# Kernel tuning notes

Hardware: AMD Instinct MI355X
Metric: run time of the kernel (lower is better)

Reference implementation:

```python
import jax, jax.numpy as jnp
import numpy as np

DIM = 1024
N_HEADS = 16
HEAD_DIM = DIM // N_HEADS
D_LATENT = 256
B, T = 1, 4096


def setup_inputs() -> dict:
    key = jax.random.key(0)
    ks = jax.random.split(key, 6)
    s = 0.02
    return {
        "x": jax.random.normal(ks[0], (B, T, DIM), dtype=jnp.float32),
        "W_DKV": jax.random.normal(ks[1], (DIM, D_LATENT), dtype=jnp.float32) * s,
        "W_UK": jax.random.normal(ks[2], (D_LATENT, DIM), dtype=jnp.float32) * s,
        "W_UV": jax.random.normal(ks[3], (D_LATENT, DIM), dtype=jnp.float32) * s,
        "W_UQ": jax.random.normal(ks[4], (DIM, DIM), dtype=jnp.float32) * s,
        "W_O": jax.random.normal(ks[5], (DIM, DIM), dtype=jnp.float32) * s,
    }


def reference(x, W_DKV, W_UK, W_UV, W_UQ, W_O):
    b, t, d = x.shape
    h, hd = N_HEADS, HEAD_DIM
    # low-rank latent KV projection
    c_kv = x @ W_DKV                                   # (b, t, d_latent)
    k = (c_kv @ W_UK).reshape(b, t, h, hd)             # (b, t, h, hd)
    v = (c_kv @ W_UV).reshape(b, t, h, hd)
    q = (x @ W_UQ).reshape(b, t, h, hd)
    scale = 1.0 / jnp.sqrt(jnp.asarray(hd, x.dtype))
    scores = jnp.einsum("bqhd,bkhd->bhqk", q, k) * scale   # (b, h, t, t)
    causal = jnp.tril(jnp.ones((t, t), dtype=bool))
    scores = jnp.where(causal, scores, jnp.asarray(-jnp.inf, scores.dtype))
    probs = jax.nn.softmax(scores, axis=-1)            # dropout is eval-mode identity
    ctx = jnp.einsum("bhqk,bkhd->bqhd", probs, v).reshape(b, t, d)
    return ctx @ W_O
```

## Files before the change

kernel.cpp:

```cpp
#include <hip/hip_runtime.h>
#include <hip/hip_bf16.h>
#include <stdint.h>

#define T_SEQ 4096
#define DIMX 1024
#define NH 16
#define HD 64
#define DLAT 256

typedef __bf16 bf16x8 __attribute__((ext_vector_type(8)));
typedef float floatx4 __attribute__((ext_vector_type(4)));

#define MFMA(a, b, c) __builtin_amdgcn_mfma_f32_16x16x32_bf16(a, b, c, 0, 0, 0)

__global__ __launch_bounds__(256) void prep_kernel(
    const float* __restrict__ x, const float* __restrict__ wdkv,
    const float* __restrict__ wuk, const float* __restrict__ wuv,
    const float* __restrict__ wuq, const float* __restrict__ wo,
    __bf16* __restrict__ x_bf, __bf16* __restrict__ wt_dkv,
    __bf16* __restrict__ wt_uk, __bf16* __restrict__ wt_uv,
    __bf16* __restrict__ wt_uq, __bf16* __restrict__ wt_o) {
  int id = blockIdx.x;
  if (id < 2048) {
    int i = id * 256 + threadIdx.x;
    const float4* p = (const float4*)x;
    float4 a = p[2 * i], b = p[2 * i + 1];
    bf16x8 r = {(__bf16)a.x, (__bf16)a.y, (__bf16)a.z, (__bf16)a.w,
                (__bf16)b.x, (__bf16)b.y, (__bf16)b.z, (__bf16)b.w};
    *(bf16x8*)(x_bf + 8 * (size_t)i) = r;
    return;
  }
  int t = id - 2048;
  const float* in;
  __bf16* out;
  int R, C, lt;
  if (t < 64)       { in = wdkv; out = wt_dkv; R = 1024; C = 256;  lt = t; }
  else if (t < 128) { in = wuk;  out = wt_uk;  R = 256;  C = 1024; lt = t - 64; }
  else if (t < 192) { in = wuv;  out = wt_uv;  R = 256;  C = 1024; lt = t - 128; }
  else if (t < 448) { in = wuq;  out = wt_uq;  R = 1024; C = 1024; lt = t - 192; }
  else              { in = wo;   out = wt_o;   R = 1024; C = 1024; lt = t - 448; }
  __shared__ __bf16 tls[64][65];
  int tpr = C >> 6;
  int r0 = (lt / tpr) * 64, c0 = (lt % tpr) * 64;
  int tid = threadIdx.x;
#pragma unroll
  for (int i = 0; i < 16; i++) {
    int idx = tid + i * 256;
    int r = idx >> 6, c = idx & 63;
    tls[r][c] = (__bf16)in[(size_t)(r0 + r) * C + c0 + c];
  }
  __syncthreads();
#pragma unroll
  for (int i = 0; i < 16; i++) {
    int idx = tid + i * 256;
    int rr = idx & 63, cc = idx >> 6;
    out[(size_t)(c0 + cc) * R + r0 + rr] = tls[rr][cc];
  }
}

#define ASTR 56
__global__ __launch_bounds__(256) void gemm_a(const __bf16* __restrict__ A,
                                              const __bf16* __restrict__ B1,
                                              const __bf16* __restrict__ B2,
                                              __bf16* __restrict__ C1,
                                              __bf16* __restrict__ C2) {
  __shared__ __attribute__((aligned(16))) __bf16 Al[64 * ASTR];
  __shared__ __attribute__((aligned(16))) __bf16 Bl[64 * ASTR];
  int tid = threadIdx.x;
  int wave = tid >> 6, lane = tid & 63;
  int quad = lane >> 4, l16 = lane & 15;
  int bx = blockIdx.x, m0 = blockIdx.y * 64;
  const __bf16* Bt;
  __bf16* C;
  int n0, N;
  float sc;
  if (bx < 4) { Bt = B1; C = C1; n0 = bx * 64; N = DLAT; sc = 1.0f; }
  else        { Bt = B2; C = C2; n0 = (bx - 4) * 64; N = DIMX; sc = 0.125f; }
  int srow = tid >> 2, skc = (tid & 3) << 3;
  const int K = DIMX;

  floatx4 acc[4];
#pragma unroll
  for (int i = 0; i < 4; i++) acc[i] = (floatx4){0.f, 0.f, 0.f, 0.f};
  const __bf16* Ap = A + (size_t)(m0 + srow) * K + skc;
  const __bf16* Bp = Bt + (size_t)(n0 + srow) * K + skc;
  for (int k0 = 0; k0 < K; k0 += 32) {
    *(bf16x8*)&Al[srow * ASTR + skc] = *(const bf16x8*)(Ap + k0);
    *(bf16x8*)&Bl[srow * ASTR + skc] = *(const bf16x8*)(Bp + k0);
    __syncthreads();
    bf16x8 af = *(const bf16x8*)&Al[(wave * 16 + l16) * ASTR + quad * 8];
#pragma unroll
    for (int nt = 0; nt < 4; nt++) {
      bf16x8 bfr = *(const bf16x8*)&Bl[(nt * 16 + l16) * ASTR + quad * 8];
      acc[nt] = MFMA(af, bfr, acc[nt]);
    }
    __syncthreads();
  }
#pragma unroll
  for (int nt = 0; nt < 4; nt++)
#pragma unroll
    for (int r = 0; r < 4; r++) {
      int row = m0 + wave * 16 + quad * 4 + r;
      int col = n0 + nt * 16 + l16;
      C[(size_t)row * N + col] = (__bf16)(acc[nt][r] * sc);
    }
}

__global__ __launch_bounds__(256) void gemm_kv(const __bf16* __restrict__ A,
                                               const __bf16* __restrict__ Bk,
                                               const __bf16* __restrict__ Bv,
                                               __bf16* __restrict__ k,
                                               __bf16* __restrict__ vt) {
  __shared__ __attribute__((aligned(16))) __bf16 Al[64 * ASTR];
  __shared__ __attribute__((aligned(16))) __bf16 Bl[64 * ASTR];
  __shared__ __attribute__((aligned(16))) __bf16 tt[64 * 72];
  int tid = threadIdx.x;
  int wave = tid >> 6, lane = tid & 63;
  int quad = lane >> 4, l16 = lane & 15;
  int bx = blockIdx.x, m0 = blockIdx.y * 64;
  bool is_k = (bx < 16);
  const __bf16* Bt = is_k ? Bk : Bv;
  int n0 = (is_k ? bx : bx - 16) * 64;
  int srow = tid >> 2, skc = (tid & 3) << 3;
  const int K = DLAT;

  floatx4 acc[4];
#pragma unroll
  for (int i = 0; i < 4; i++) acc[i] = (floatx4){0.f, 0.f, 0.f, 0.f};
  const __bf16* Ap = A + (size_t)(m0 + srow) * K + skc;
  const __bf16* Bp = Bt + (size_t)(n0 + srow) * K + skc;
  for (int k0 = 0; k0 < K; k0 += 32) {
    *(bf16x8*)&Al[srow * ASTR + skc] = *(const bf16x8*)(Ap + k0);
    *(bf16x8*)&Bl[srow * ASTR + skc] = *(const bf16x8*)(Bp + k0);
    __syncthreads();
    bf16x8 af = *(const bf16x8*)&Al[(wave * 16 + l16) * ASTR + quad * 8];
#pragma unroll
    for (int nt = 0; nt < 4; nt++) {
      bf16x8 bfr = *(const bf16x8*)&Bl[(nt * 16 + l16) * ASTR + quad * 8];
      acc[nt] = MFMA(af, bfr, acc[nt]);
    }
    __syncthreads();
  }
  if (is_k) {
#pragma unroll
    for (int nt = 0; nt < 4; nt++)
#pragma unroll
      for (int r = 0; r < 4; r++) {
        int row = m0 + wave * 16 + quad * 4 + r;
        int col = n0 + nt * 16 + l16;
        k[(size_t)row * DIMX + col] = (__bf16)acc[nt][r];
      }
  } else {
#pragma unroll
    for (int nt = 0; nt < 4; nt++)
#pragma unroll
      for (int r = 0; r < 4; r++)
        tt[(nt * 16 + l16) * 72 + wave * 16 + quad * 4 + r] = (__bf16)acc[nt][r];
    __syncthreads();
#pragma unroll
    for (int i = 0; i < 2; i++) {
      int idx = tid + i * 256;
      int cc = idx >> 3, rr = (idx & 7) << 3;
      *(bf16x8*)&vt[(size_t)(n0 + cc) * T_SEQ + m0 + rr] =
          *(const bf16x8*)&tt[cc * 72 + rr];
    }
  }
}

#define PST 72
__global__ __launch_bounds__(512, 4) void mla_attn5(const __bf16* __restrict__ Q,
                                                    const __bf16* __restrict__ Kg,
                                                    const __bf16* __restrict__ Vt,
                                                    __bf16* __restrict__ ctx) {
  __shared__ __attribute__((aligned(16))) __bf16 Kl[2][64 * 64];
  __shared__ __attribute__((aligned(16))) __bf16 Vl[2][64 * 64];
  __shared__ __attribute__((aligned(16))) __bf16 Pl[128 * PST];
  int tid = threadIdx.x;
  int wave = tid >> 6, lane = tid & 63;
  int quad = lane >> 4, l16 = lane & 15;
  int wq = wave & 3;
  bool isA = (wave < 4);
  int qa = blockIdx.x, h = blockIdx.y;
  int qb = 63 - qa;
  int myqt = isA ? qa : qb;
  int myq0 = myqt * 64;
  int srow = tid >> 3, pos = tid & 7;
  int gco = pos << 3;
  int sw = ((pos ^ (srow & 7)) << 3);
  int swr = srow * 64 + sw;

  *(bf16x8*)&Pl[srow * PST + gco] =
      *(const bf16x8*)&Q[(size_t)(qa * 64 + srow) * DIMX + h * HD + gco];
  *(bf16x8*)&Pl[(64 + srow) * PST + gco] =
      *(const bf16x8*)&Q[(size_t)(qb * 64 + srow) * DIMX + h * HD + gco];
  *(bf16x8*)&Kl[0][swr] =
      *(const bf16x8*)&Kg[(size_t)srow * DIMX + h * HD + gco];
  *(bf16x8*)&Vl[0][swr] =
      *(const bf16x8*)&Vt[(size_t)(h * HD + srow) * T_SEQ + gco];
  __syncthreads();
  int fr = (wave * 16 + l16) * PST;
  bf16x8 qf0 = *(const bf16x8*)&Pl[fr + quad * 8];
  bf16x8 qf1 = *(const bf16x8*)&Pl[fr + 32 + quad * 8];

  int c0s = ((quad ^ (l16 & 7)) << 3);
  int c1s = (((4 + quad) ^ (l16 & 7)) << 3);

  floatx4 o[4];
  float l_i[4];
#pragma unroll
  for (int i = 0; i < 4; i++) {
    o[i] = (floatx4){0.f, 0.f, 0.f, 0.f};
    l_i[i] = 0.f;
  }

  for (int kt = 0; kt <= qb; kt++) {
    int cur = kt & 1, nxt = cur ^ 1;
    bool pre = (kt < qb);
    bf16x8 kpre, vpre;
    if (pre) {
      int k0n = (kt + 1) * 64;
      kpre = *(const bf16x8*)&Kg[(size_t)(k0n + srow) * DIMX + h * HD + gco];
      vpre = *(const bf16x8*)&Vt[(size_t)(h * HD + srow) * T_SEQ + k0n + gco];
    }
    if (!isA || kt <= qa) {
      const __bf16* Kc = Kl[cur];
      const __bf16* Vc = Vl[cur];
      floatx4 s[4];
#pragma unroll
      for (int ct = 0; ct < 4; ct++) {
        int rb = (ct * 16 + l16) * 64;
        bf16x8 kf0 = *(const bf16x8*)&Kc[rb + c0s];
        bf16x8 kf1 = *(const bf16x8*)&Kc[rb + c1s];
        floatx4 z = (floatx4){0.f, 0.f, 0.f, 0.f};
        z = MFMA(qf0, kf0, z);
        z = MFMA(qf1, kf1, z);
        s[ct] = z;
      }
      bool diag = (kt == myqt);
#pragma unroll
      for (int ct = 0; ct < 4; ct++)
#pragma unroll
        for (int r = 0; r < 4; r++) {
          float p = __expf(s[ct][r]);
          if (diag && (ct * 16 + l16 > wq * 16 + quad * 4 + r)) p = 0.f;
          l_i[r] += p;
          Pl[(wave * 16 + quad * 4 + r) * PST + ct * 16 + l16] = (__bf16)p;
        }
      bf16x8 pf0 = *(const bf16x8*)&Pl[fr + quad * 8];
      bf16x8 pf1 = *(const bf16x8*)&Pl[fr + 32 + quad * 8];
#pragma unroll
      for (int dt = 0; dt < 4; dt++) {
        int rb = (dt * 16 + l16) * 64;
        bf16x8 vf0 = *(const bf16x8*)&Vc[rb + c0s];
        bf16x8 vf1 = *(const bf16x8*)&Vc[rb + c1s];
        o[dt] = MFMA(pf0, vf0, o[dt]);
        o[dt] = MFMA(pf1, vf1, o[dt]);
      }
    }
    if (pre) {
      *(bf16x8*)&Kl[nxt][swr] = kpre;
      *(bf16x8*)&Vl[nxt][swr] = vpre;
    }
    __syncthreads();
  }

#pragma unroll
  for (int off = 1; off < 16; off <<= 1)
#pragma unroll
    for (int r = 0; r < 4; r++) l_i[r] += __shfl_xor(l_i[r], off, 64);

#pragma unroll
  for (int dt = 0; dt < 4; dt++)
#pragma unroll
    for (int r = 0; r < 4; r++) {
      float val = o[dt][r] / l_i[r];
      int row = myq0 + wq * 16 + quad * 4 + r;
      int col = h * HD + dt * 16 + l16;
      ctx[(size_t)row * DIMX + col] = (__bf16)val;
    }
}

__global__ __launch_bounds__(256) void gemm_f(const __bf16* __restrict__ A,
                                              const __bf16* __restrict__ Bt,
                                              float* __restrict__ C,
                                              int M, int N, int K) {
  __shared__ __attribute__((aligned(16))) __bf16 Al[64 * ASTR];
  __shared__ __attribute__((aligned(16))) __bf16 Bl[64 * ASTR];
  int tid = threadIdx.x;
  int wave = tid >> 6, lane = tid & 63;
  int quad = lane >> 4, l16 = lane & 15;
  int n0 = blockIdx.x * 64, m0 = blockIdx.y * 64;
  int srow = tid >> 2, skc = (tid & 3) << 3;

  floatx4 acc[4];
#pragma unroll
  for (int i = 0; i < 4; i++) acc[i] = (floatx4){0.f, 0.f, 0.f, 0.f};
  const __bf16* Ap = A + (size_t)(m0 + srow) * K + skc;
  const __bf16* Bp = Bt + (size_t)(n0 + srow) * K + skc;
  for (int k0 = 0; k0 < K; k0 += 32) {
    *(bf16x8*)&Al[srow * ASTR + skc] = *(const bf16x8*)(Ap + k0);
    *(bf16x8*)&Bl[srow * ASTR + skc] = *(const bf16x8*)(Bp + k0);
    __syncthreads();
    bf16x8 af = *(const bf16x8*)&Al[(wave * 16 + l16) * ASTR + quad * 8];
#pragma unroll
    for (int nt = 0; nt < 4; nt++) {
      bf16x8 bfr = *(const bf16x8*)&Bl[(nt * 16 + l16) * ASTR + quad * 8];
      acc[nt] = MFMA(af, bfr, acc[nt]);
    }
    __syncthreads();
  }
#pragma unroll
  for (int nt = 0; nt < 4; nt++)
#pragma unroll
    for (int r = 0; r < 4; r++) {
      int row = m0 + wave * 16 + quad * 4 + r;
      int col = n0 + nt * 16 + l16;
      C[(size_t)row * N + col] = acc[nt][r];
    }
}

extern "C" void kernel_launch(void* const* d_in, const int* in_sizes, int n_in,
                              void* d_out, int out_size, void* d_ws,
                              size_t ws_size, hipStream_t stream) {
  const float* x = (const float*)d_in[0];
  const float* wdkv = (const float*)d_in[1];
  const float* wuk = (const float*)d_in[2];
  const float* wuv = (const float*)d_in[3];
  const float* wuq = (const float*)d_in[4];
  const float* wo = (const float*)d_in[5];
  float* out = (float*)d_out;

  __bf16* ws = (__bf16*)d_ws;
  __bf16* x_bf = ws;
  __bf16* q = x_bf + (size_t)T_SEQ * DIMX;
  __bf16* k = q + (size_t)T_SEQ * DIMX;
  __bf16* vt = k + (size_t)T_SEQ * DIMX;
  __bf16* ctx = vt + (size_t)T_SEQ * DIMX;
  __bf16* ckv = ctx + (size_t)T_SEQ * DIMX;
  __bf16* wt_dkv = ckv + (size_t)T_SEQ * DLAT;
  __bf16* wt_uk = wt_dkv + (size_t)DLAT * DIMX;
  __bf16* wt_uv = wt_uk + (size_t)DIMX * DLAT;
  __bf16* wt_uq = wt_uv + (size_t)DIMX * DLAT;
  __bf16* wt_o = wt_uq + (size_t)DIMX * DIMX;

  dim3 blk(256);
  prep_kernel<<<dim3(2752), blk, 0, stream>>>(x, wdkv, wuk, wuv, wuq, wo, x_bf,
                                              wt_dkv, wt_uk, wt_uv, wt_uq, wt_o);
  gemm_a<<<dim3(20, T_SEQ / 64), blk, 0, stream>>>(x_bf, wt_dkv, wt_uq, ckv, q);
  gemm_kv<<<dim3(32, T_SEQ / 64), blk, 0, stream>>>(ckv, wt_uk, wt_uv, k, vt);
  mla_attn5<<<dim3(32, NH), dim3(512), 0, stream>>>(q, k, vt, ctx);
  gemm_f<<<dim3(DIMX / 64, T_SEQ / 64), blk, 0, stream>>>(ctx, wt_o, out, T_SEQ,
                                                          DIMX, DIMX);
}
```

Baseline: 230.2 us.

## Retile projection GEMMs to 128x128 with direct global-to-LDS loads

Replaces the 64x64-tile GEMMs for the latent/query, K/V and output projections with 128x128 tiles where each wave computes a 64x64 sub-tile via 16 MFMAs per k-step. Operand tiles are staged with global_load_lds, bypassing registers. The aim is more arithmetic reuse per loaded byte and fewer load instructions. It also reverses the query-tile order for half the heads in the attention kernel to spread causal work, at the cost of unpadded LDS (possible bank conflicts), more registers and fewer blocks per grid.

```diff
diff --git a/kernel.cpp b/kernel.cpp
--- a/kernel.cpp
+++ b/kernel.cpp
@@ -12,6 +12,12 @@
 typedef float floatx4 __attribute__((ext_vector_type(4)));
 
 #define MFMA(a, b, c) __builtin_amdgcn_mfma_f32_16x16x32_bf16(a, b, c, 0, 0, 0)
+
+__device__ inline void gload_lds16(const __bf16* g, __bf16* l) {
+  __builtin_amdgcn_global_load_lds(
+      (const __attribute__((address_space(1))) uint32_t*)g,
+      (__attribute__((address_space(3))) uint32_t*)l, 16, 0, 0);
+}
 
 __global__ __launch_bounds__(256) void prep_kernel(
     const float* __restrict__ x, const float* __restrict__ wdkv,
@@ -58,113 +64,200 @@
   }
 }
 
-#define ASTR 56
-__global__ __launch_bounds__(256) void gemm_a(const __bf16* __restrict__ A,
-                                              const __bf16* __restrict__ B1,
-                                              const __bf16* __restrict__ B2,
-                                              __bf16* __restrict__ C1,
-                                              __bf16* __restrict__ C2) {
-  __shared__ __attribute__((aligned(16))) __bf16 Al[64 * ASTR];
-  __shared__ __attribute__((aligned(16))) __bf16 Bl[64 * ASTR];
+
+__global__ __launch_bounds__(256) void gemm_a128(const __bf16* __restrict__ A,
+                                                 const __bf16* __restrict__ B1,
+                                                 const __bf16* __restrict__ B2,
+                                                 __bf16* __restrict__ C1,
+                                                 __bf16* __restrict__ C2) {
+  __shared__ __attribute__((aligned(16))) __bf16 Al[128 * 32];
+  __shared__ __attribute__((aligned(16))) __bf16 Bl[128 * 32];
   int tid = threadIdx.x;
-  int wave = tid >> 6, lane = tid & 63;
+  int w = tid >> 6, lane = tid & 63;
   int quad = lane >> 4, l16 = lane & 15;
-  int bx = blockIdx.x, m0 = blockIdx.y * 64;
+  int mw = w & 1, nw = w >> 1;
+  int bx = blockIdx.x, m0 = blockIdx.y * 128;
   const __bf16* Bt;
   __bf16* C;
   int n0, N;
   float sc;
-  if (bx < 4) { Bt = B1; C = C1; n0 = bx * 64; N = DLAT; sc = 1.0f; }
-  else        { Bt = B2; C = C2; n0 = (bx - 4) * 64; N = DIMX; sc = 0.125f; }
-  int srow = tid >> 2, skc = (tid & 3) << 3;
+  if (bx < 2) { Bt = B1; C = C1; n0 = bx * 128; N = DLAT; sc = 1.0f; }
+  else        { Bt = B2; C = C2; n0 = (bx - 2) * 128; N = DIMX; sc = 0.125f; }
   const int K = DIMX;
-
-  floatx4 acc[4];
-#pragma unroll
-  for (int i = 0; i < 4; i++) acc[i] = (floatx4){0.f, 0.f, 0.f, 0.f};
-  const __bf16* Ap = A + (size_t)(m0 + srow) * K + skc;
-  const __bf16* Bp = Bt + (size_t)(n0 + srow) * K + skc;
+  int arow = w * 32 + (lane >> 2), acol = (lane & 3) << 3;
+
+  floatx4 acc[4][4];
+#pragma unroll
+  for (int i = 0; i < 4; i++)
+#pragma unroll
+    for (int j = 0; j < 4; j++) acc[i][j] = (floatx4){0.f, 0.f, 0.f, 0.f};
+
   for (int k0 = 0; k0 < K; k0 += 32) {
-    *(bf16x8*)&Al[srow * ASTR + skc] = *(const bf16x8*)(Ap + k0);
-    *(bf16x8*)&Bl[srow * ASTR + skc] = *(const bf16x8*)(Bp + k0);
-    __syncthreads();
-    bf16x8 af = *(const bf16x8*)&Al[(wave * 16 + l16) * ASTR + quad * 8];
-#pragma unroll
-    for (int nt = 0; nt < 4; nt++) {
-      bf16x8 bfr = *(const bf16x8*)&Bl[(nt * 16 + l16) * ASTR + quad * 8];
-      acc[nt] = MFMA(af, bfr, acc[nt]);
-    }
-    __syncthreads();
-  }
-#pragma unroll
-  for (int nt = 0; nt < 4; nt++)
-#pragma unroll
-    for (int r = 0; r < 4; r++) {
-      int row = m0 + wave * 16 + quad * 4 + r;
-      int col = n0 + nt * 16 + l16;
-      C[(size_t)row * N + col] = (__bf16)(acc[nt][r] * sc);
-    }
-}
-
-__global__ __launch_bounds__(256) void gemm_kv(const __bf16* __restrict__ A,
-                                               const __bf16* __restrict__ Bk,
-                                               const __bf16* __restrict__ Bv,
-                                               __bf16* __restrict__ k,
-                                               __bf16* __restrict__ vt) {
-  __shared__ __attribute__((aligned(16))) __bf16 Al[64 * ASTR];
-  __shared__ __attribute__((aligned(16))) __bf16 Bl[64 * ASTR];
-  __shared__ __attribute__((aligned(16))) __bf16 tt[64 * 72];
+#pragma unroll
+    for (int j = 0; j < 2; j++) {
+      gload_lds16(A + (size_t)(m0 + arow + j * 16) * K + k0 + acol,
+                  &Al[(w * 32 + j * 16) * 32]);
+      gload_lds16(Bt + (size_t)(n0 + arow + j * 16) * K + k0 + acol,
+                  &Bl[(w * 32 + j * 16) * 32]);
+    }
+    __syncthreads();
+    bf16x8 af[4], bfr[4];
+#pragma unroll
+    for (int mt = 0; mt < 4; mt++)
+      af[mt] = *(const bf16x8*)&Al[(mw * 64 + mt * 16 + l16) * 32 + quad * 8];
+#pragma unroll
+    for (int nt = 0; nt < 4; nt++)
+      bfr[nt] = *(const bf16x8*)&Bl[(nw * 64 + nt * 16 + l16) * 32 + quad * 8];
+#pragma unroll
+    for (int mt = 0; mt < 4; mt++)
+#pragma unroll
+      for (int nt = 0; nt < 4; nt++)
+        acc[mt][nt] = MFMA(af[mt], bfr[nt], acc[mt][nt]);
+    __syncthreads();
+  }
+#pragma unroll
+  for (int mt = 0; mt < 4; mt++)
+#pragma unroll
+    for (int nt = 0; nt < 4; nt++)
+#pragma unroll
+      for (int r = 0; r < 4; r++) {
+        int row = m0 + mw * 64 + mt * 16 + quad * 4 + r;
+        int col = n0 + nw * 64 + nt * 16 + l16;
+        C[(size_t)row * N + col] = (__bf16)(acc[mt][nt][r] * sc);
+      }
+}
+
+__global__ __launch_bounds__(256) void gemm_kv128(const __bf16* __restrict__ A,
+                                                  const __bf16* __restrict__ Bk,
+                                                  const __bf16* __restrict__ Bv,
+                                                  __bf16* __restrict__ k,
+                                                  __bf16* __restrict__ vt) {
+  __shared__ __attribute__((aligned(16))) __bf16 Al[128 * 32];
+  __shared__ __attribute__((aligned(16))) __bf16 Bl[128 * 32];
+  __shared__ __attribute__((aligned(16))) __bf16 tw[4][64 * 72];
   int tid = threadIdx.x;
-  int wave = tid >> 6, lane = tid & 63;
+  int w = tid >> 6, lane = tid & 63;
   int quad = lane >> 4, l16 = lane & 15;
-  int bx = blockIdx.x, m0 = blockIdx.y * 64;
-  bool is_k = (bx < 16);
+  int mw = w & 1, nw = w >> 1;
+  int bx = blockIdx.x, m0 = blockIdx.y * 128;
+  bool is_k = (bx < 8);
   const __bf16* Bt = is_k ? Bk : Bv;
-  int n0 = (is_k ? bx : bx - 16) * 64;
-  int srow = tid >> 2, skc = (tid & 3) << 3;
+  int n0 = (is_k ? bx : bx - 8) * 128;
   const int K = DLAT;
-
-  floatx4 acc[4];
-#pragma unroll
-  for (int i = 0; i < 4; i++) acc[i] = (floatx4){0.f, 0.f, 0.f, 0.f};
-  const __bf16* Ap = A + (size_t)(m0 + srow) * K + skc;
-  const __bf16* Bp = Bt + (size_t)(n0 + srow) * K + skc;
+  int arow = w * 32 + (lane >> 2), acol = (lane & 3) << 3;
+
+  floatx4 acc[4][4];
+#pragma unroll
+  for (int i = 0; i < 4; i++)
+#pragma unroll
+    for (int j = 0; j < 4; j++) acc[i][j] = (floatx4){0.f, 0.f, 0.f, 0.f};
+
   for (int k0 = 0; k0 < K; k0 += 32) {
-    *(bf16x8*)&Al[srow * ASTR + skc] = *(const bf16x8*)(Ap + k0);
-    *(bf16x8*)&Bl[srow * ASTR + skc] = *(const bf16x8*)(Bp + k0);
-    __syncthreads();
-    bf16x8 af = *(const bf16x8*)&Al[(wave * 16 + l16) * ASTR + quad * 8];
-#pragma unroll
-    for (int nt = 0; nt < 4; nt++) {
-      bf16x8 bfr = *(const bf16x8*)&Bl[(nt * 16 + l16) * ASTR + quad * 8];
-      acc[nt] = MFMA(af, bfr, acc[nt]);
-    }
+#pragma unroll
+    for (int j = 0; j < 2; j++) {
+      gload_lds16(A + (size_t)(m0 + arow + j * 16) * K + k0 + acol,
+                  &Al[(w * 32 + j * 16) * 32]);
+      gload_lds16(Bt + (size_t)(n0 + arow + j * 16) * K + k0 + acol,
+                  &Bl[(w * 32 + j * 16) * 32]);
+    }
+    __syncthreads();
+    bf16x8 af[4], bfr[4];
+#pragma unroll
+    for (int mt = 0; mt < 4; mt++)
+      af[mt] = *(const bf16x8*)&Al[(mw * 64 + mt * 16 + l16) * 32 + quad * 8];
+#pragma unroll
+    for (int nt = 0; nt < 4; nt++)
+      bfr[nt] = *(const bf16x8*)&Bl[(nw * 64 + nt * 16 + l16) * 32 + quad * 8];
+#pragma unroll
+    for (int mt = 0; mt < 4; mt++)
+#pragma unroll
+      for (int nt = 0; nt < 4; nt++)
+        acc[mt][nt] = MFMA(af[mt], bfr[nt], acc[mt][nt]);
     __syncthreads();
   }
   if (is_k) {
 #pragma unroll
+    for (int mt = 0; mt < 4; mt++)
+#pragma unroll
+      for (int nt = 0; nt < 4; nt++)
+#pragma unroll
+        for (int r = 0; r < 4; r++) {
+          int row = m0 + mw * 64 + mt * 16 + quad * 4 + r;
+          int col = n0 + nw * 64 + nt * 16 + l16;
+          k[(size_t)row * DIMX + col] = (__bf16)acc[mt][nt][r];
+        }
+  } else {
+#pragma unroll
+    for (int mt = 0; mt < 4; mt++)
+#pragma unroll
+      for (int nt = 0; nt < 4; nt++)
+#pragma unroll
+        for (int r = 0; r < 4; r++)
+          tw[w][(nt * 16 + l16) * 72 + mt * 16 + quad * 4 + r] =
+              (__bf16)acc[mt][nt][r];
+    int cbase = lane >> 3, chunk = lane & 7;
+#pragma unroll
+    for (int i = 0; i < 8; i++) {
+      int c = cbase + i * 8;
+      bf16x8 v8 = *(const bf16x8*)&tw[w][c * 72 + chunk * 8];
+      *(bf16x8*)&vt[(size_t)(n0 + nw * 64 + c) * T_SEQ + m0 + mw * 64 +
+                    chunk * 8] = v8;
+    }
+  }
+}
+
+__global__ __launch_bounds__(256) void gemm_f128(const __bf16* __restrict__ A,
+                                                 const __bf16* __restrict__ Bt,
+                                                 float* __restrict__ C) {
+  __shared__ __attribute__((aligned(16))) __bf16 Al[128 * 32];
+  __shared__ __attribute__((aligned(16))) __bf16 Bl[128 * 32];
+  int tid = threadIdx.x;
+  int w = tid >> 6, lane = tid & 63;
+  int quad = lane >> 4, l16 = lane & 15;
+  int mw = w & 1, nw = w >> 1;
+  int n0 = blockIdx.x * 128, m0 = blockIdx.y * 128;
+  const int K = DIMX, N = DIMX;
+  int arow = w * 32 + (lane >> 2), acol = (lane & 3) << 3;
+
+  floatx4 acc[4][4];
+#pragma unroll
+  for (int i = 0; i < 4; i++)
+#pragma unroll
+    for (int j = 0; j < 4; j++) acc[i][j] = (floatx4){0.f, 0.f, 0.f, 0.f};
+
+  for (int k0 = 0; k0 < K; k0 += 32) {
+#pragma unroll
+    for (int j = 0; j < 2; j++) {
+      gload_lds16(A + (size_t)(m0 + arow + j * 16) * K + k0 + acol,
+                  &Al[(w * 32 + j * 16) * 32]);
+      gload_lds16(Bt + (size_t)(n0 + arow + j * 16) * K + k0 + acol,
+                  &Bl[(w * 32 + j * 16) * 32]);
+    }
+    __syncthreads();
+    bf16x8 af[4], bfr[4];
+#pragma unroll
+    for (int mt = 0; mt < 4; mt++)
+      af[mt] = *(const bf16x8*)&Al[(mw * 64 + mt * 16 + l16) * 32 + quad * 8];
+#pragma unroll
     for (int nt = 0; nt < 4; nt++)
+      bfr[nt] = *(const bf16x8*)&Bl[(nw * 64 + nt * 16 + l16) * 32 + quad * 8];
+#pragma unroll
+    for (int mt = 0; mt < 4; mt++)
+#pragma unroll
+      for (int nt = 0; nt < 4; nt++)
+        acc[mt][nt] = MFMA(af[mt], bfr[nt], acc[mt][nt]);
+    __syncthreads();
+  }
+#pragma unroll
+  for (int mt = 0; mt < 4; mt++)
+#pragma unroll
+    for (int nt = 0; nt < 4; nt++)
 #pragma unroll
       for (int r = 0; r < 4; r++) {
-        int row = m0 + wave * 16 + quad * 4 + r;
-        int col = n0 + nt * 16 + l16;
-        k[(size_t)row * DIMX + col] = (__bf16)acc[nt][r];
+        int row = m0 + mw * 64 + mt * 16 + quad * 4 + r;
+        int col = n0 + nw * 64 + nt * 16 + l16;
+        C[(size_t)row * N + col] = acc[mt][nt][r];
       }
-  } else {
-#pragma unroll
-    for (int nt = 0; nt < 4; nt++)
-#pragma unroll
-      for (int r = 0; r < 4; r++)
-        tt[(nt * 16 + l16) * 72 + wave * 16 + quad * 4 + r] = (__bf16)acc[nt][r];
-    __syncthreads();
-#pragma unroll
-    for (int i = 0; i < 2; i++) {
-      int idx = tid + i * 256;
-      int cc = idx >> 3, rr = (idx & 7) << 3;
-      *(bf16x8*)&vt[(size_t)(n0 + cc) * T_SEQ + m0 + rr] =
-          *(const bf16x8*)&tt[cc * 72 + rr];
-    }
-  }
 }
 
 #define PST 72
@@ -180,7 +273,8 @@
   int quad = lane >> 4, l16 = lane & 15;
   int wq = wave & 3;
   bool isA = (wave < 4);
-  int qa = blockIdx.x, h = blockIdx.y;
+  int h = blockIdx.y;
+  int qa = (h & 8) ? (31 - blockIdx.x) : blockIdx.x;
   int qb = 63 - qa;
   int myqt = isA ? qa : qb;
   int myq0 = myqt * 64;
@@ -280,45 +374,6 @@
     }
 }
 
-__global__ __launch_bounds__(256) void gemm_f(const __bf16* __restrict__ A,
-                                              const __bf16* __restrict__ Bt,
-                                              float* __restrict__ C,
-                                              int M, int N, int K) {
-  __shared__ __attribute__((aligned(16))) __bf16 Al[64 * ASTR];
-  __shared__ __attribute__((aligned(16))) __bf16 Bl[64 * ASTR];
-  int tid = threadIdx.x;
-  int wave = tid >> 6, lane = tid & 63;
-  int quad = lane >> 4, l16 = lane & 15;
-  int n0 = blockIdx.x * 64, m0 = blockIdx.y * 64;
-  int srow = tid >> 2, skc = (tid & 3) << 3;
-
-  floatx4 acc[4];
-#pragma unroll
-  for (int i = 0; i < 4; i++) acc[i] = (floatx4){0.f, 0.f, 0.f, 0.f};
-  const __bf16* Ap = A + (size_t)(m0 + srow) * K + skc;
-  const __bf16* Bp = Bt + (size_t)(n0 + srow) * K + skc;
-  for (int k0 = 0; k0 < K; k0 += 32) {
-    *(bf16x8*)&Al[srow * ASTR + skc] = *(const bf16x8*)(Ap + k0);
-    *(bf16x8*)&Bl[srow * ASTR + skc] = *(const bf16x8*)(Bp + k0);
-    __syncthreads();
-    bf16x8 af = *(const bf16x8*)&Al[(wave * 16 + l16) * ASTR + quad * 8];
-#pragma unroll
-    for (int nt = 0; nt < 4; nt++) {
-      bf16x8 bfr = *(const bf16x8*)&Bl[(nt * 16 + l16) * ASTR + quad * 8];
-      acc[nt] = MFMA(af, bfr, acc[nt]);
-    }
-    __syncthreads();
-  }
-#pragma unroll
-  for (int nt = 0; nt < 4; nt++)
-#pragma unroll
-    for (int r = 0; r < 4; r++) {
-      int row = m0 + wave * 16 + quad * 4 + r;
-      int col = n0 + nt * 16 + l16;
-      C[(size_t)row * N + col] = acc[nt][r];
-    }
-}
-
 extern "C" void kernel_launch(void* const* d_in, const int* in_sizes, int n_in,
                               void* d_out, int out_size, void* d_ws,
                               size_t ws_size, hipStream_t stream) {
@@ -346,9 +401,10 @@
   dim3 blk(256);
   prep_kernel<<<dim3(2752), blk, 0, stream>>>(x, wdkv, wuk, wuv, wuq, wo, x_bf,
                                               wt_dkv, wt_uk, wt_uv, wt_uq, wt_o);
-  gemm_a<<<dim3(20, T_SEQ / 64), blk, 0, stream>>>(x_bf, wt_dkv, wt_uq, ckv, q);
-  gemm_kv<<<dim3(32, T_SEQ / 64), blk, 0, stream>>>(ckv, wt_uk, wt_uv, k, vt);
+  gemm_a128<<<dim3(10, T_SEQ / 128), blk, 0, stream>>>(x_bf, wt_dkv, wt_uq,
+                                                       ckv, q);
+  gemm_kv128<<<dim3(16, T_SEQ / 128), blk, 0, stream>>>(ckv, wt_uk, wt_uv, k,
+                                                        vt);
   mla_attn5<<<dim3(32, NH), dim3(512), 0, stream>>>(q, k, vt, ctx);
-  gemm_f<<<dim3(DIMX / 64, T_SEQ / 64), blk, 0, stream>>>(ctx, wt_o, out, T_SEQ,
-                                                          DIMX, DIMX);
-}
+  gemm_f128<<<dim3(DIMX / 128, T_SEQ / 128), blk, 0, stream>>>(ctx, wt_o, out);
+}
```

Result: faster. 214.1 us (-7.0%).
